# Kernel tuning notes

Hardware: AMD Instinct MI355X
Metric: run time of the kernel (lower is better)

## Reference

```python
import jax, jax.numpy as jnp
import numpy as np

DIM = 768
NUM_HEADS = 12
HEAD_DIM = DIM // NUM_HEADS
SCALE = HEAD_DIM ** -0.5


def setup_inputs() -> dict:
    key = jax.random.key(0)
    k1, k2, k3, k4, k5 = jax.random.split(key, 5)
    B, N, C = 4, 1024, DIM
    x = jax.random.normal(k1, (B, N, C), dtype=jnp.float32)
    # padding mask: last quarter of tokens masked out for half the batch
    mask = jnp.ones((B, N), dtype=bool)
    mask = mask.at[B // 2:, 3 * N // 4:].set(False)
    w_qkv = jax.random.normal(k2, (3 * C, C), dtype=jnp.float32) * (C ** -0.5)
    w_proj = jax.random.normal(k3, (C, C), dtype=jnp.float32) * (C ** -0.5)
    b_proj = jax.random.normal(k4, (C,), dtype=jnp.float32) * 0.02
    return {"x": x, "mask": mask, "w_qkv": w_qkv, "w_proj": w_proj, "b_proj": b_proj}


def reference(x, mask, w_qkv, w_proj, b_proj):
    B, N, C = x.shape
    H, D = NUM_HEADS, HEAD_DIM
    # qkv: Linear without bias -> [B, N, 3C] -> [3, B, H, N, D]
    qkv = jnp.einsum('bnc,oc->bno', x, w_qkv).reshape(B, N, 3, H, D)
    qkv = jnp.transpose(qkv, (2, 0, 3, 1, 4))
    q, k, v = qkv[0], qkv[1], qkv[2]
    attn = jnp.einsum('bhnd,bhmd->bhnm', q, k) * SCALE  # [B,H,N,N]
    # outer-product padding mask: mask[:,None,:] * mask[:,:,None], broadcast over heads
    pair_mask = (mask[:, None, :] & mask[:, :, None])[:, None, :, :]  # [B,1,N,N]
    mask_value = -jnp.finfo(attn.dtype).max
    attn = jnp.where(pair_mask, attn, mask_value)
    attn = jax.nn.softmax(attn, axis=-1)
    out = jnp.einsum('bhnm,bhmd->bhnd', attn, v)  # [B,H,N,D]
    out = jnp.transpose(out, (0, 2, 1, 3)).reshape(B, N, C)
    out = jnp.einsum('bnc,oc->bno', out, w_proj) + b_proj
    return out
```

## Files before the change

### kernel.cpp

```cpp
#include <hip/hip_runtime.h>
#include <hip/hip_fp16.h>
#include <float.h>

typedef _Float16 f16;
typedef __attribute__((ext_vector_type(4))) _Float16 f16x4;
typedef __attribute__((ext_vector_type(8))) _Float16 f16x8;
typedef __attribute__((ext_vector_type(4))) float f32x4;

#define NB 4
#define SEQ 1024
#define DIM 768
#define NH 12
#define HD 64
#define SCALE_F 0.125f
#define LOG2E 1.44269504088896f
#define NBH (NB * NH)
#define MASK_NEG (-1.0e30f)

__device__ __forceinline__ void gload16(const f16* g, f16* lds) {
    __builtin_amdgcn_global_load_lds(
        (const __attribute__((address_space(1))) void*)g,
        (__attribute__((address_space(3))) void*)lds, 16, 0, 0);
}

__global__ __launch_bounds__(256) void cvt_mask_kernel(
    const float* __restrict__ X, const float* __restrict__ W1,
    const float* __restrict__ W2, const void* __restrict__ mask_raw,
    f16* __restrict__ Xh, f16* __restrict__ W1h, f16* __restrict__ W2h,
    float* __restrict__ Mb) {
    const int A4 = (NB * SEQ * DIM) / 4;
    const int B4 = (3 * DIM * DIM) / 4;
    const int C4 = (DIM * DIM) / 4;
    const int tid = threadIdx.x;
    if (blockIdx.x == (unsigned)(A4 + B4 + C4 + 255) / 256) {
        __shared__ int is_u8;
        if (tid == 0) is_u8 = 0;
        __syncthreads();
        const unsigned int* u32 = (const unsigned int*)mask_raw;
        int bad = 0;
        for (int i = tid; i < (NB * SEQ) / 4; i += 256)
            if (u32[i] > 1u) bad = 1;
        if (bad) atomicOr(&is_u8, 1);
        __syncthreads();
        const int u8mode = is_u8;
        const unsigned char* u8 = (const unsigned char*)mask_raw;
        const int* i32 = (const int*)mask_raw;
        for (int i = tid; i < NB * SEQ; i += 256) {
            const int m = u8mode ? (u8[i] != 0) : (i32[i] != 0);
            Mb[i] = m ? 0.0f : MASK_NEG;
        }
        return;
    }
    int i = blockIdx.x * 256 + tid;
    const float* s; f16* d; int j;
    if (i < A4)                { s = X;  d = Xh;  j = i; }
    else if (i < A4 + B4)      { s = W1; d = W1h; j = i - A4; }
    else if (i < A4 + B4 + C4) { s = W2; d = W2h; j = i - A4 - B4; }
    else return;
    float4 v = ((const float4*)s)[j];
    f16x4 h;
    h[0] = (f16)v.x; h[1] = (f16)v.y; h[2] = (f16)v.z; h[3] = (f16)v.w;
    *(f16x4*)(d + 4 * (size_t)j) = h;
}

__global__ __launch_bounds__(256) void qkv_gemm_f16(
    const f16* __restrict__ Xh, const f16* __restrict__ Wh,
    f16* __restrict__ Qh, f16* __restrict__ Kh, f16* __restrict__ Vth) {
    __shared__ __align__(16) f16 Ah[2][128 * 32];
    __shared__ __align__(16) f16 Bh[2][128 * 32];
    const int tid = threadIdx.x;
    const int l = tid & 63, w = tid >> 6;
    const int lo = l & 15, hi = l >> 4;
    const int wm = w >> 1, wn = w & 1;
    const int m0 = blockIdx.y * 128, o0 = blockIdx.x * 128;

    f32x4 acc[4][4];
#pragma unroll
    for (int i = 0; i < 4; ++i)
#pragma unroll
        for (int j = 0; j < 4; ++j) { f32x4 z = {0.f, 0.f, 0.f, 0.f}; acc[i][j] = z; }

    const int gr = l >> 2;
    const int gc = (l & 3) * 8;
    const f16* gA = Xh + (size_t)(m0 + w * 32 + gr) * DIM + gc;
    const f16* gB = Wh + (size_t)(o0 + w * 32 + gr) * DIM + gc;
    const int lofs = (w * 2) * 512;

    gload16(gA,            Ah[0] + lofs);
    gload16(gA + 16 * DIM, Ah[0] + lofs + 512);
    gload16(gB,            Bh[0] + lofs);
    gload16(gB + 16 * DIM, Bh[0] + lofs + 512);
    __syncthreads();

    int cur = 0;
    for (int k0 = 0; k0 < DIM; k0 += 32) {
        if (k0 + 32 < DIM) {
            gload16(gA + k0 + 32,            Ah[cur ^ 1] + lofs);
            gload16(gA + k0 + 32 + 16 * DIM, Ah[cur ^ 1] + lofs + 512);
            gload16(gB + k0 + 32,            Bh[cur ^ 1] + lofs);
            gload16(gB + k0 + 32 + 16 * DIM, Bh[cur ^ 1] + lofs + 512);
        }
        f16x8 af[4], bf[4];
#pragma unroll
        for (int i = 0; i < 4; ++i)
            af[i] = *(const f16x8*)&Ah[cur][(wm * 64 + i * 16 + lo) * 32 + hi * 8];
#pragma unroll
        for (int j = 0; j < 4; ++j)
            bf[j] = *(const f16x8*)&Bh[cur][(wn * 64 + j * 16 + lo) * 32 + hi * 8];
#pragma unroll
        for (int i = 0; i < 4; ++i)
#pragma unroll
            for (int j = 0; j < 4; ++j)
                acc[i][j] = __builtin_amdgcn_mfma_f32_16x16x32_f16(af[i], bf[j], acc[i][j], 0, 0, 0);
        __syncthreads();
        cur ^= 1;
    }

    const int oo = o0 + wn * 64;
    const int s = oo / DIM;
    const int hh = (oo % DIM) / HD;
    const int b = m0 >> 10;
    const int nbase = (m0 & 1023) + wm * 64;
    if (s < 2) {
        f16* dst = (s == 0) ? Qh : Kh;
        const float qs = (s == 0) ? SCALE_F * LOG2E : 1.0f;
        f16* base = dst + ((size_t)(b * NH + hh)) * SEQ * HD;
#pragma unroll
        for (int i = 0; i < 4; ++i)
#pragma unroll
            for (int r = 0; r < 4; ++r) {
                const int n = nbase + i * 16 + hi * 4 + r;
#pragma unroll
                for (int j = 0; j < 4; ++j)
                    base[(size_t)n * HD + j * 16 + lo] = (f16)(acc[i][j][r] * qs);
            }
    } else {
        f16* base = Vth + ((size_t)(b * NH + hh)) * HD * SEQ;
#pragma unroll
        for (int i = 0; i < 4; ++i) {
            const int n4 = nbase + i * 16 + hi * 4;
#pragma unroll
            for (int j = 0; j < 4; ++j) {
                const int d = j * 16 + lo;
                f16x4 pv;
#pragma unroll
                for (int r = 0; r < 4; ++r) pv[r] = (f16)acc[i][j][r];
                *(f16x4*)(base + (size_t)d * SEQ + n4) = pv;
            }
        }
    }
}

__global__ __launch_bounds__(256) void attn_f16(
    const f16* __restrict__ Qh, const f16* __restrict__ Kh,
    const f16* __restrict__ Vth, const float* __restrict__ Mb,
    f16* __restrict__ Oh) {
    const int bh = blockIdx.y, b = bh / NH, hh = bh % NH;
    const int q0 = blockIdx.x * 64;
    const int tid = threadIdx.x;
    const int l = tid & 63, w = tid >> 6;
    const int lo = l & 15, hi = l >> 4;

    __shared__ __align__(16) f16 Ks[2][64][64];
    __shared__ __align__(16) f16 Vs[2][64][64];
    __shared__ __align__(16) f16 Ps[4][16][64];

    const f16* Qp = Qh + (size_t)bh * SEQ * HD;
    const f16* Kp = Kh + (size_t)bh * SEQ * HD;
    const f16* Vp = Vth + (size_t)bh * HD * SEQ;
    const float* Mbb = Mb + b * SEQ;

    f16x8 qa[2];
#pragma unroll
    for (int kk = 0; kk < 2; ++kk)
        qa[kk] = *(const f16x8*)(Qp + (size_t)(q0 + w * 16 + lo) * HD + kk * 32 + hi * 8);
    const bool mq = (Mbb[q0 + w * 16 + lo] == 0.0f);

    float m_run = -FLT_MAX, l_run = 0.f;
    f32x4 oacc[4];
#pragma unroll
    for (int n = 0; n < 4; ++n) { f32x4 z = {0.f, 0.f, 0.f, 0.f}; oacc[n] = z; }

    const int sr = tid >> 2, sc = (tid & 3) * 16;
    const int swz = (sr & 7) * 8;
    const int s8 = (lo & 7) * 8;

    f16x8 kr0, kr1, vr0, vr1;
    kr0 = *(const f16x8*)(Kp + (size_t)sr * HD + sc);
    kr1 = *(const f16x8*)(Kp + (size_t)sr * HD + sc + 8);
    vr0 = *(const f16x8*)(Vp + (size_t)sr * SEQ + sc);
    vr1 = *(const f16x8*)(Vp + (size_t)sr * SEQ + sc + 8);
    *(f16x8*)&Ks[0][sr][sc ^ swz]       = kr0;
    *(f16x8*)&Ks[0][sr][(sc + 8) ^ swz] = kr1;
    *(f16x8*)&Vs[0][sr][sc ^ swz]       = vr0;
    *(f16x8*)&Vs[0][sr][(sc + 8) ^ swz] = vr1;
    kr0 = *(const f16x8*)(Kp + (size_t)(64 + sr) * HD + sc);
    kr1 = *(const f16x8*)(Kp + (size_t)(64 + sr) * HD + sc + 8);
    vr0 = *(const f16x8*)(Vp + (size_t)sr * SEQ + 64 + sc);
    vr1 = *(const f16x8*)(Vp + (size_t)sr * SEQ + 64 + sc + 8);
    __syncthreads();

    int cur = 0;
    for (int t = 0; t < SEQ / 64; ++t) {
        const int kv0 = t * 64;
        f32x4 sf[4];
#pragma unroll
        for (int f = 0; f < 4; ++f) { f32x4 z = {0.f, 0.f, 0.f, 0.f}; sf[f] = z; }
#pragma unroll
        for (int kk = 0; kk < 2; ++kk)
#pragma unroll
            for (int f = 0; f < 4; ++f) {
                f16x8 kf = *(const f16x8*)&Ks[cur][f * 16 + lo][(kk * 32 + hi * 8) ^ s8];
                sf[f] = __builtin_amdgcn_mfma_f32_16x16x32_f16(kf, qa[kk], sf[f], 0, 0, 0);
            }
        if (t < SEQ / 64 - 1) {
            *(f16x8*)&Ks[cur ^ 1][sr][sc ^ swz]       = kr0;
            *(f16x8*)&Ks[cur ^ 1][sr][(sc + 8) ^ swz] = kr1;
            *(f16x8*)&Vs[cur ^ 1][sr][sc ^ swz]       = vr0;
            *(f16x8*)&Vs[cur ^ 1][sr][(sc + 8) ^ swz] = vr1;
            if (t < SEQ / 64 - 2) {
                const int kv2 = kv0 + 128;
                kr0 = *(const f16x8*)(Kp + (size_t)(kv2 + sr) * HD + sc);
                kr1 = *(const f16x8*)(Kp + (size_t)(kv2 + sr) * HD + sc + 8);
                vr0 = *(const f16x8*)(Vp + (size_t)sr * SEQ + kv2 + sc);
                vr1 = *(const f16x8*)(Vp + (size_t)sr * SEQ + kv2 + sc + 8);
            }
        }
        f32x4 bias[4];
#pragma unroll
        for (int f = 0; f < 4; ++f)
            bias[f] = *(const f32x4*)(Mbb + kv0 + f * 16 + hi * 4);
#pragma unroll
        for (int f = 0; f < 4; ++f)
#pragma unroll
            for (int r = 0; r < 4; ++r) {
                const float sv = sf[f][r] + bias[f][r];
                sf[f][r] = mq ? sv : 0.0f;
            }
        float pm = -FLT_MAX;
#pragma unroll
        for (int f = 0; f < 4; ++f)
            pm = fmaxf(pm, fmaxf(fmaxf(sf[f][0], sf[f][1]), fmaxf(sf[f][2], sf[f][3])));
        pm = fmaxf(pm, __shfl_xor(pm, 16));
        pm = fmaxf(pm, __shfl_xor(pm, 32));
        const float mn = fmaxf(m_run, pm);
        const float alpha = exp2f(m_run - mn);
        m_run = mn;
        float rs = 0.f;
#pragma unroll
        for (int f = 0; f < 4; ++f)
#pragma unroll
            for (int r = 0; r < 4; ++r) {
                float p = exp2f(sf[f][r] - mn);
                sf[f][r] = p;
                rs += p;
            }
        rs += __shfl_xor(rs, 16);
        rs += __shfl_xor(rs, 32);
        l_run = l_run * alpha + rs;

#pragma unroll
        for (int f = 0; f < 4; ++f) {
            f16x4 pv;
#pragma unroll
            for (int r = 0; r < 4; ++r) pv[r] = (f16)sf[f][r];
            *(f16x4*)&Ps[w][lo][(f * 16 + hi * 4) ^ s8] = pv;
        }
        if (!__all(alpha == 1.0f)) {
            float ar[4];
#pragma unroll
            for (int r = 0; r < 4; ++r) ar[r] = __shfl(alpha, hi * 4 + r);
#pragma unroll
            for (int n = 0; n < 4; ++n)
#pragma unroll
                for (int r = 0; r < 4; ++r) oacc[n][r] *= ar[r];
        }
#pragma unroll
        for (int kk = 0; kk < 2; ++kk) {
            f16x8 pa = *(const f16x8*)&Ps[w][lo][(kk * 32 + hi * 8) ^ s8];
#pragma unroll
            for (int n = 0; n < 4; ++n) {
                f16x8 vb = *(const f16x8*)&Vs[cur][n * 16 + lo][(kk * 32 + hi * 8) ^ s8];
                oacc[n] = __builtin_amdgcn_mfma_f32_16x16x32_f16(pa, vb, oacc[n], 0, 0, 0);
            }
        }
        __syncthreads();
        cur ^= 1;
    }

    float il[4];
#pragma unroll
    for (int r = 0; r < 4; ++r) il[r] = __shfl(l_run, hi * 4 + r);
    f16* Op = Oh + ((size_t)b * SEQ + q0 + w * 16) * DIM + hh * HD;
#pragma unroll
    for (int r = 0; r < 4; ++r) {
        const float inv = 1.f / il[r];
#pragma unroll
        for (int n = 0; n < 4; ++n)
            Op[(size_t)(hi * 4 + r) * DIM + n * 16 + lo] = (f16)(oacc[n][r] * inv);
    }
}

__global__ __launch_bounds__(256) void proj_gemm_f16(
    const f16* __restrict__ Oh, const f16* __restrict__ Wph,
    const float* __restrict__ bp, float* __restrict__ out) {
    __shared__ __align__(16) f16 Ah[2][128 * 32];
    __shared__ __align__(16) f16 Bh[2][128 * 32];
    const int tid = threadIdx.x;
    const int l = tid & 63, w = tid >> 6;
    const int lo = l & 15, hi = l >> 4;
    const int wm = w >> 1, wn = w & 1;
    const int m0 = blockIdx.y * 128, o0 = blockIdx.x * 128;

    f32x4 acc[4][4];
#pragma unroll
    for (int i = 0; i < 4; ++i)
#pragma unroll
        for (int j = 0; j < 4; ++j) { f32x4 z = {0.f, 0.f, 0.f, 0.f}; acc[i][j] = z; }

    const int gr = l >> 2;
    const int gc = (l & 3) * 8;
    const f16* gA = Oh + (size_t)(m0 + w * 32 + gr) * DIM + gc;
    const f16* gB = Wph + (size_t)(o0 + w * 32 + gr) * DIM + gc;
    const int lofs = (w * 2) * 512;

    gload16(gA,            Ah[0] + lofs);
    gload16(gA + 16 * DIM, Ah[0] + lofs + 512);
    gload16(gB,            Bh[0] + lofs);
    gload16(gB + 16 * DIM, Bh[0] + lofs + 512);
    __syncthreads();

    int cur = 0;
    for (int k0 = 0; k0 < DIM; k0 += 32) {
        if (k0 + 32 < DIM) {
            gload16(gA + k0 + 32,            Ah[cur ^ 1] + lofs);
            gload16(gA + k0 + 32 + 16 * DIM, Ah[cur ^ 1] + lofs + 512);
            gload16(gB + k0 + 32,            Bh[cur ^ 1] + lofs);
            gload16(gB + k0 + 32 + 16 * DIM, Bh[cur ^ 1] + lofs + 512);
        }
        f16x8 af[4], bf[4];
#pragma unroll
        for (int i = 0; i < 4; ++i)
            af[i] = *(const f16x8*)&Ah[cur][(wm * 64 + i * 16 + lo) * 32 + hi * 8];
#pragma unroll
        for (int j = 0; j < 4; ++j)
            bf[j] = *(const f16x8*)&Bh[cur][(wn * 64 + j * 16 + lo) * 32 + hi * 8];
#pragma unroll
        for (int i = 0; i < 4; ++i)
#pragma unroll
            for (int j = 0; j < 4; ++j)
                acc[i][j] = __builtin_amdgcn_mfma_f32_16x16x32_f16(af[i], bf[j], acc[i][j], 0, 0, 0);
        __syncthreads();
        cur ^= 1;
    }

    float bpv[4];
#pragma unroll
    for (int j = 0; j < 4; ++j) bpv[j] = bp[o0 + wn * 64 + j * 16 + lo];
#pragma unroll
    for (int i = 0; i < 4; ++i)
#pragma unroll
        for (int r = 0; r < 4; ++r) {
            const int m = m0 + wm * 64 + i * 16 + hi * 4 + r;
#pragma unroll
            for (int j = 0; j < 4; ++j)
                out[(size_t)m * DIM + o0 + wn * 64 + j * 16 + lo] = acc[i][j][r] + bpv[j];
        }
}

extern "C" void kernel_launch(void* const* d_in, const int* in_sizes, int n_in,
                              void* d_out, int out_size, void* d_ws, size_t ws_size,
                              hipStream_t stream) {
    const float* x      = (const float*)d_in[0];
    const void*  mask   = d_in[1];
    const float* w_qkv  = (const float*)d_in[2];
    const float* w_proj = (const float*)d_in[3];
    const float* b_proj = (const float*)d_in[4];
    float* out          = (float*)d_out;

    char* w = (char*)d_ws;
    float* Mb = (float*)w;                 w += 16384;
    const size_t NX  = (size_t)NB * SEQ * DIM;
    const size_t NW1 = (size_t)3 * DIM * DIM;
    const size_t NW2 = (size_t)DIM * DIM;
    f16* Xh   = (f16*)w;  w += NX  * sizeof(f16);
    f16* W1h  = (f16*)w;  w += NW1 * sizeof(f16);
    f16* W2h  = (f16*)w;  w += NW2 * sizeof(f16);
    f16* Qh   = (f16*)w;  w += NX * sizeof(f16);
    f16* Kh   = (f16*)w;  w += NX * sizeof(f16);
    f16* Vth  = (f16*)w;  w += NX * sizeof(f16);
    f16* Oh   = (f16*)w;  w += NX * sizeof(f16);

    const int cvt_blocks = ((NB * SEQ * DIM + 4 * DIM * DIM) / 4 + 255) / 256 + 1;
    cvt_mask_kernel<<<cvt_blocks, 256, 0, stream>>>(x, w_qkv, w_proj, mask,
                                                    Xh, W1h, W2h, Mb);
    qkv_gemm_f16<<<dim3(18, 32), 256, 0, stream>>>(Xh, W1h, Qh, Kh, Vth);
    attn_f16<<<dim3(SEQ / 64, NBH), 256, 0, stream>>>(Qh, Kh, Vth, Mb, Oh);
    proj_gemm_f16<<<dim3(6, 32), 256, 0, stream>>>(Oh, W2h, b_proj, out);
}
```

Measured before the change: 97.11 us.

## Skip mask bias for unmasked KV tiles, remap attention blocks, raise MFMA priority

The mask-conversion kernel now also writes a per-64-token tile flag that records whether any token in the tile is masked. The attention kernel reads this flag and skips the bias load and add for fully unmasked KV tiles, and skips the query-row select when every query in the wave is valid. The attention grid is flattened to 1D with a block-index remap, likely to place blocks on XCDs so those sharing a head share K/V in cache. s_setprio is raised around the MFMA sections. Together this trims per-tile ALU and global loads at the cost of a few extra atomics and a flag read per tile.

New measurement: 101.7 us. +4.7%, slower.

```diff
diff --git a/kernel.cpp b/kernel.cpp
--- a/kernel.cpp
+++ b/kernel.cpp
@@ -27,7 +27,7 @@
     const float* __restrict__ X, const float* __restrict__ W1,
     const float* __restrict__ W2, const void* __restrict__ mask_raw,
     f16* __restrict__ Xh, f16* __restrict__ W1h, f16* __restrict__ W2h,
-    float* __restrict__ Mb) {
+    float* __restrict__ Mb, int* __restrict__ TF) {
     const int A4 = (NB * SEQ * DIM) / 4;
     const int B4 = (3 * DIM * DIM) / 4;
     const int C4 = (DIM * DIM) / 4;
@@ -35,6 +35,7 @@
     if (blockIdx.x == (unsigned)(A4 + B4 + C4 + 255) / 256) {
         __shared__ int is_u8;
         if (tid == 0) is_u8 = 0;
+        if (tid < NB * 16) TF[tid] = 0;
         __syncthreads();
         const unsigned int* u32 = (const unsigned int*)mask_raw;
         int bad = 0;
@@ -48,6 +49,7 @@
         for (int i = tid; i < NB * SEQ; i += 256) {
             const int m = u8mode ? (u8[i] != 0) : (i32[i] != 0);
             Mb[i] = m ? 0.0f : MASK_NEG;
+            if (!m) atomicOr(&TF[i >> 6], 1);
         }
         return;
     }
@@ -154,9 +156,11 @@
 __global__ __launch_bounds__(256) void attn_f16(
     const f16* __restrict__ Qh, const f16* __restrict__ Kh,
     const f16* __restrict__ Vth, const float* __restrict__ Mb,
-    f16* __restrict__ Oh) {
-    const int bh = blockIdx.y, b = bh / NH, hh = bh % NH;
-    const int q0 = blockIdx.x * 64;
+    const int* __restrict__ TF, f16* __restrict__ Oh) {
+    const int bid = blockIdx.x;
+    const int swz = (bid & 7) * 96 + (bid >> 3);
+    const int bh = swz >> 4, b = bh / NH, hh = bh % NH;
+    const int q0 = (swz & 15) * 64;
     const int tid = threadIdx.x;
     const int l = tid & 63, w = tid >> 6;
     const int lo = l & 15, hi = l >> 4;
@@ -169,12 +173,14 @@
     const f16* Kp = Kh + (size_t)bh * SEQ * HD;
     const f16* Vp = Vth + (size_t)bh * HD * SEQ;
     const float* Mbb = Mb + b * SEQ;
+    const int* TFb = TF + b * 16;
 
     f16x8 qa[2];
 #pragma unroll
     for (int kk = 0; kk < 2; ++kk)
         qa[kk] = *(const f16x8*)(Qp + (size_t)(q0 + w * 16 + lo) * HD + kk * 32 + hi * 8);
     const bool mq = (Mbb[q0 + w * 16 + lo] == 0.0f);
+    const bool all_mq = __all(mq);
 
     float m_run = -FLT_MAX, l_run = 0.f;
     f32x4 oacc[4];
@@ -182,7 +188,7 @@
     for (int n = 0; n < 4; ++n) { f32x4 z = {0.f, 0.f, 0.f, 0.f}; oacc[n] = z; }
 
     const int sr = tid >> 2, sc = (tid & 3) * 16;
-    const int swz = (sr & 7) * 8;
+    const int swl = (sr & 7) * 8;
     const int s8 = (lo & 7) * 8;
 
     f16x8 kr0, kr1, vr0, vr1;
@@ -190,10 +196,10 @@
     kr1 = *(const f16x8*)(Kp + (size_t)sr * HD + sc + 8);
     vr0 = *(const f16x8*)(Vp + (size_t)sr * SEQ + sc);
     vr1 = *(const f16x8*)(Vp + (size_t)sr * SEQ + sc + 8);
-    *(f16x8*)&Ks[0][sr][sc ^ swz]       = kr0;
-    *(f16x8*)&Ks[0][sr][(sc + 8) ^ swz] = kr1;
-    *(f16x8*)&Vs[0][sr][sc ^ swz]       = vr0;
-    *(f16x8*)&Vs[0][sr][(sc + 8) ^ swz] = vr1;
+    *(f16x8*)&Ks[0][sr][sc ^ swl]       = kr0;
+    *(f16x8*)&Ks[0][sr][(sc + 8) ^ swl] = kr1;
+    *(f16x8*)&Vs[0][sr][sc ^ swl]       = vr0;
+    *(f16x8*)&Vs[0][sr][(sc + 8) ^ swl] = vr1;
     kr0 = *(const f16x8*)(Kp + (size_t)(64 + sr) * HD + sc);
     kr1 = *(const f16x8*)(Kp + (size_t)(64 + sr) * HD + sc + 8);
     vr0 = *(const f16x8*)(Vp + (size_t)sr * SEQ + 64 + sc);
@@ -206,6 +212,7 @@
         f32x4 sf[4];
 #pragma unroll
         for (int f = 0; f < 4; ++f) { f32x4 z = {0.f, 0.f, 0.f, 0.f}; sf[f] = z; }
+        __builtin_amdgcn_s_setprio(1);
 #pragma unroll
         for (int kk = 0; kk < 2; ++kk)
 #pragma unroll
@@ -213,11 +220,12 @@
                 f16x8 kf = *(const f16x8*)&Ks[cur][f * 16 + lo][(kk * 32 + hi * 8) ^ s8];
                 sf[f] = __builtin_amdgcn_mfma_f32_16x16x32_f16(kf, qa[kk], sf[f], 0, 0, 0);
             }
+        __builtin_amdgcn_s_setprio(0);
         if (t < SEQ / 64 - 1) {
-            *(f16x8*)&Ks[cur ^ 1][sr][sc ^ swz]       = kr0;
-            *(f16x8*)&Ks[cur ^ 1][sr][(sc + 8) ^ swz] = kr1;
-            *(f16x8*)&Vs[cur ^ 1][sr][sc ^ swz]       = vr0;
-            *(f16x8*)&Vs[cur ^ 1][sr][(sc + 8) ^ swz] = vr1;
+            *(f16x8*)&Ks[cur ^ 1][sr][sc ^ swl]       = kr0;
+            *(f16x8*)&Ks[cur ^ 1][sr][(sc + 8) ^ swl] = kr1;
+            *(f16x8*)&Vs[cur ^ 1][sr][sc ^ swl]       = vr0;
+            *(f16x8*)&Vs[cur ^ 1][sr][(sc + 8) ^ swl] = vr1;
             if (t < SEQ / 64 - 2) {
                 const int kv2 = kv0 + 128;
                 kr0 = *(const f16x8*)(Kp + (size_t)(kv2 + sr) * HD + sc);
@@ -226,17 +234,21 @@
                 vr1 = *(const f16x8*)(Vp + (size_t)sr * SEQ + kv2 + sc + 8);
             }
         }
-        f32x4 bias[4];
-#pragma unroll
-        for (int f = 0; f < 4; ++f)
-            bias[f] = *(const f32x4*)(Mbb + kv0 + f * 16 + hi * 4);
-#pragma unroll
-        for (int f = 0; f < 4; ++f)
-#pragma unroll
-            for (int r = 0; r < 4; ++r) {
-                const float sv = sf[f][r] + bias[f][r];
-                sf[f][r] = mq ? sv : 0.0f;
-            }
+        const int any_mkv = TFb[t];
+        if (any_mkv) {
+#pragma unroll
+            for (int f = 0; f < 4; ++f) {
+                f32x4 bias = *(const f32x4*)(Mbb + kv0 + f * 16 + hi * 4);
+#pragma unroll
+                for (int r = 0; r < 4; ++r) sf[f][r] += bias[r];
+            }
+        }
+        if (!all_mq) {
+#pragma unroll
+            for (int f = 0; f < 4; ++f)
+#pragma unroll
+                for (int r = 0; r < 4; ++r) sf[f][r] = mq ? sf[f][r] : 0.0f;
+        }
         float pm = -FLT_MAX;
 #pragma unroll
         for (int f = 0; f < 4; ++f)
@@ -275,6 +287,7 @@
 #pragma unroll
                 for (int r = 0; r < 4; ++r) oacc[n][r] *= ar[r];
         }
+        __builtin_amdgcn_s_setprio(1);
 #pragma unroll
         for (int kk = 0; kk < 2; ++kk) {
             f16x8 pa = *(const f16x8*)&Ps[w][lo][(kk * 32 + hi * 8) ^ s8];
@@ -284,6 +297,7 @@
                 oacc[n] = __builtin_amdgcn_mfma_f32_16x16x32_f16(pa, vb, oacc[n], 0, 0, 0);
             }
         }
+        __builtin_amdgcn_s_setprio(0);
         __syncthreads();
         cur ^= 1;
     }
@@ -379,7 +393,8 @@
     float* out          = (float*)d_out;
 
     char* w = (char*)d_ws;
-    float* Mb = (float*)w;                 w += 16384;
+    float* Mb = (float*)w;                 w += NB * SEQ * sizeof(float);
+    int* TF   = (int*)w;                   w += 256;
     const size_t NX  = (size_t)NB * SEQ * DIM;
     const size_t NW1 = (size_t)3 * DIM * DIM;
     const size_t NW2 = (size_t)DIM * DIM;
@@ -393,8 +408,8 @@
 
     const int cvt_blocks = ((NB * SEQ * DIM + 4 * DIM * DIM) / 4 + 255) / 256 + 1;
     cvt_mask_kernel<<<cvt_blocks, 256, 0, stream>>>(x, w_qkv, w_proj, mask,
-                                                    Xh, W1h, W2h, Mb);
+                                                    Xh, W1h, W2h, Mb, TF);
     qkv_gemm_f16<<<dim3(18, 32), 256, 0, stream>>>(Xh, W1h, Qh, Kh, Vth);
-    attn_f16<<<dim3(SEQ / 64, NBH), 256, 0, stream>>>(Qh, Kh, Vth, Mb, Oh);
+    attn_f16<<<dim3(768), 256, 0, stream>>>(Qh, Kh, Vth, Mb, TF, Oh);
     proj_gemm_f16<<<dim3(6, 32), 256, 0, stream>>>(Oh, W2h, b_proj, out);
 }
```

## Split attention KV loop across two blocks and add a combine kernel

Applied to the files above, without the earlier changes.

The attention kernel gains a third grid dimension that splits the 1024-key sequence into two halves. Each block writes unnormalized f16 partial outputs plus per-row running max and sum to workspace. A new combine kernel rescales the two partials, normalizes them and writes the final head-interleaved output. The aim is to double the number of attention blocks and shorten each block's serial KV loop for better CU fill, at the cost of an extra launch, extra global traffic for the partials, and f16 rounding of the unnormalized accumulators.

New measurement: 101.3 us. 1.04x slower.

```diff
diff --git a/kernel.cpp b/kernel.cpp
--- a/kernel.cpp
+++ b/kernel.cpp
@@ -16,6 +16,8 @@
 #define LOG2E 1.44269504088896f
 #define NBH (NB * NH)
 #define MASK_NEG (-1.0e30f)
+#define KVSPLIT 2
+#define ROWS ((size_t)NBH * SEQ)
 
 __device__ __forceinline__ void gload16(const f16* g, f16* lds) {
     __builtin_amdgcn_global_load_lds(
@@ -154,9 +156,10 @@
 __global__ __launch_bounds__(256) void attn_f16(
     const f16* __restrict__ Qh, const f16* __restrict__ Kh,
     const f16* __restrict__ Vth, const float* __restrict__ Mb,
-    f16* __restrict__ Oh) {
-    const int bh = blockIdx.y, b = bh / NH, hh = bh % NH;
+    f16* __restrict__ Po, float* __restrict__ Pml) {
+    const int bh = blockIdx.y, b = bh / NH;
     const int q0 = blockIdx.x * 64;
+    const int kvb = blockIdx.z * (SEQ / KVSPLIT);
     const int tid = threadIdx.x;
     const int l = tid & 63, w = tid >> 6;
     const int lo = l & 15, hi = l >> 4;
@@ -182,27 +185,28 @@
     for (int n = 0; n < 4; ++n) { f32x4 z = {0.f, 0.f, 0.f, 0.f}; oacc[n] = z; }
 
     const int sr = tid >> 2, sc = (tid & 3) * 16;
-    const int swz = (sr & 7) * 8;
+    const int swl = (sr & 7) * 8;
     const int s8 = (lo & 7) * 8;
 
     f16x8 kr0, kr1, vr0, vr1;
-    kr0 = *(const f16x8*)(Kp + (size_t)sr * HD + sc);
-    kr1 = *(const f16x8*)(Kp + (size_t)sr * HD + sc + 8);
-    vr0 = *(const f16x8*)(Vp + (size_t)sr * SEQ + sc);
-    vr1 = *(const f16x8*)(Vp + (size_t)sr * SEQ + sc + 8);
-    *(f16x8*)&Ks[0][sr][sc ^ swz]       = kr0;
-    *(f16x8*)&Ks[0][sr][(sc + 8) ^ swz] = kr1;
-    *(f16x8*)&Vs[0][sr][sc ^ swz]       = vr0;
-    *(f16x8*)&Vs[0][sr][(sc + 8) ^ swz] = vr1;
-    kr0 = *(const f16x8*)(Kp + (size_t)(64 + sr) * HD + sc);
-    kr1 = *(const f16x8*)(Kp + (size_t)(64 + sr) * HD + sc + 8);
-    vr0 = *(const f16x8*)(Vp + (size_t)sr * SEQ + 64 + sc);
-    vr1 = *(const f16x8*)(Vp + (size_t)sr * SEQ + 64 + sc + 8);
+    kr0 = *(const f16x8*)(Kp + (size_t)(kvb + sr) * HD + sc);
+    kr1 = *(const f16x8*)(Kp + (size_t)(kvb + sr) * HD + sc + 8);
+    vr0 = *(const f16x8*)(Vp + (size_t)sr * SEQ + kvb + sc);
+    vr1 = *(const f16x8*)(Vp + (size_t)sr * SEQ + kvb + sc + 8);
+    *(f16x8*)&Ks[0][sr][sc ^ swl]       = kr0;
+    *(f16x8*)&Ks[0][sr][(sc + 8) ^ swl] = kr1;
+    *(f16x8*)&Vs[0][sr][sc ^ swl]       = vr0;
+    *(f16x8*)&Vs[0][sr][(sc + 8) ^ swl] = vr1;
+    kr0 = *(const f16x8*)(Kp + (size_t)(kvb + 64 + sr) * HD + sc);
+    kr1 = *(const f16x8*)(Kp + (size_t)(kvb + 64 + sr) * HD + sc + 8);
+    vr0 = *(const f16x8*)(Vp + (size_t)sr * SEQ + kvb + 64 + sc);
+    vr1 = *(const f16x8*)(Vp + (size_t)sr * SEQ + kvb + 64 + sc + 8);
     __syncthreads();
 
+    const int NT = SEQ / KVSPLIT / 64;
     int cur = 0;
-    for (int t = 0; t < SEQ / 64; ++t) {
-        const int kv0 = t * 64;
+    for (int t = 0; t < NT; ++t) {
+        const int kv0 = kvb + t * 64;
         f32x4 sf[4];
 #pragma unroll
         for (int f = 0; f < 4; ++f) { f32x4 z = {0.f, 0.f, 0.f, 0.f}; sf[f] = z; }
@@ -213,12 +217,12 @@
                 f16x8 kf = *(const f16x8*)&Ks[cur][f * 16 + lo][(kk * 32 + hi * 8) ^ s8];
                 sf[f] = __builtin_amdgcn_mfma_f32_16x16x32_f16(kf, qa[kk], sf[f], 0, 0, 0);
             }
-        if (t < SEQ / 64 - 1) {
-            *(f16x8*)&Ks[cur ^ 1][sr][sc ^ swz]       = kr0;
-            *(f16x8*)&Ks[cur ^ 1][sr][(sc + 8) ^ swz] = kr1;
-            *(f16x8*)&Vs[cur ^ 1][sr][sc ^ swz]       = vr0;
-            *(f16x8*)&Vs[cur ^ 1][sr][(sc + 8) ^ swz] = vr1;
-            if (t < SEQ / 64 - 2) {
+        if (t < NT - 1) {
+            *(f16x8*)&Ks[cur ^ 1][sr][sc ^ swl]       = kr0;
+            *(f16x8*)&Ks[cur ^ 1][sr][(sc + 8) ^ swl] = kr1;
+            *(f16x8*)&Vs[cur ^ 1][sr][sc ^ swl]       = vr0;
+            *(f16x8*)&Vs[cur ^ 1][sr][(sc + 8) ^ swl] = vr1;
+            if (t < NT - 2) {
                 const int kv2 = kv0 + 128;
                 kr0 = *(const f16x8*)(Kp + (size_t)(kv2 + sr) * HD + sc);
                 kr1 = *(const f16x8*)(Kp + (size_t)(kv2 + sr) * HD + sc + 8);
@@ -288,16 +292,41 @@
         cur ^= 1;
     }
 
-    float il[4];
-#pragma unroll
-    for (int r = 0; r < 4; ++r) il[r] = __shfl(l_run, hi * 4 + r);
-    f16* Op = Oh + ((size_t)b * SEQ + q0 + w * 16) * DIM + hh * HD;
-#pragma unroll
-    for (int r = 0; r < 4; ++r) {
-        const float inv = 1.f / il[r];
+    const size_t prow = (size_t)blockIdx.z * ROWS + (size_t)bh * SEQ + q0 + w * 16;
+    if (hi == 0)
+        *(float2*)&Pml[(prow + lo) * 2] = make_float2(m_run, l_run);
+    f16* Pop = Po + prow * HD;
+#pragma unroll
+    for (int r = 0; r < 4; ++r)
 #pragma unroll
         for (int n = 0; n < 4; ++n)
-            Op[(size_t)(hi * 4 + r) * DIM + n * 16 + lo] = (f16)(oacc[n][r] * inv);
+            Pop[(size_t)(hi * 4 + r) * HD + n * 16 + lo] = (f16)oacc[n][r];
+}
+
+__global__ __launch_bounds__(256) void attn_combine(
+    const f16* __restrict__ Po, const float* __restrict__ Pml,
+    f16* __restrict__ Oh) {
+    const int idx = blockIdx.x * 256 + threadIdx.x;
+    const int r4 = idx >> 2, c16 = (idx & 3) * 16;
+    const int bh = r4 >> 10, q = r4 & 1023;
+    const int b = bh / NH, hh = bh % NH;
+    const size_t base0 = (size_t)r4;
+    const size_t base1 = ROWS + (size_t)r4;
+    const float m1 = Pml[base0 * 2], l1 = Pml[base0 * 2 + 1];
+    const float m2 = Pml[base1 * 2], l2 = Pml[base1 * 2 + 1];
+    const float M = fmaxf(m1, m2);
+    const float c1 = exp2f(m1 - M), c2 = exp2f(m2 - M);
+    const float inv = 1.f / (l1 * c1 + l2 * c2);
+    const f16x8* o1 = (const f16x8*)(Po + base0 * HD + c16);
+    const f16x8* o2 = (const f16x8*)(Po + base1 * HD + c16);
+    f16* dst = Oh + ((size_t)b * SEQ + q) * DIM + hh * HD + c16;
+#pragma unroll
+    for (int h = 0; h < 2; ++h) {
+        f16x8 a = o1[h], bb = o2[h], o;
+#pragma unroll
+        for (int j = 0; j < 8; ++j)
+            o[j] = (f16)(((float)a[j] * c1 + (float)bb[j] * c2) * inv);
+        *(f16x8*)(dst + h * 8) = o;
     }
 }
 
@@ -390,11 +419,14 @@
     f16* Kh   = (f16*)w;  w += NX * sizeof(f16);
     f16* Vth  = (f16*)w;  w += NX * sizeof(f16);
     f16* Oh   = (f16*)w;  w += NX * sizeof(f16);
+    f16* Po   = (f16*)w;  w += (size_t)KVSPLIT * ROWS * HD * sizeof(f16);
+    float* Pml = (float*)w; w += (size_t)KVSPLIT * ROWS * 2 * sizeof(float);
 
     const int cvt_blocks = ((NB * SEQ * DIM + 4 * DIM * DIM) / 4 + 255) / 256 + 1;
     cvt_mask_kernel<<<cvt_blocks, 256, 0, stream>>>(x, w_qkv, w_proj, mask,
                                                     Xh, W1h, W2h, Mb);
     qkv_gemm_f16<<<dim3(18, 32), 256, 0, stream>>>(Xh, W1h, Qh, Kh, Vth);
-    attn_f16<<<dim3(SEQ / 64, NBH), 256, 0, stream>>>(Qh, Kh, Vth, Mb, Oh);
+    attn_f16<<<dim3(SEQ / 64, NBH, KVSPLIT), 256, 0, stream>>>(Qh, Kh, Vth, Mb, Po, Pml);
+    attn_combine<<<(int)(ROWS * 4 / 256), 256, 0, stream>>>(Po, Pml, Oh);
     proj_gemm_f16<<<dim3(6, 32), 256, 0, stream>>>(Oh, W2h, b_proj, out);
 }
```
